# Kernel optimization log

Hardware: AMD Instinct MI355X
Metric: run time of the kernel (lower is better)

## Reference

```python
import jax, jax.numpy as jnp
import numpy as np

B, C, H, W = 32, 48, 64, 128
K = 5  # conv kernel size (1x5 / 5x1)


def _conv1d(x, w, b):
    # x: [B, C, L]; w: [O, I, K]; b: [O]. 'same' conv (pad 2) along L.
    y = jax.lax.conv_general_dilated(x, w, window_strides=(1,), padding=[(2, 2)],
                                     dimension_numbers=("NCH", "OIH", "NCH"))
    return y + b[None, :, None]


def setup_inputs() -> dict:
    key = jax.random.key(0)
    ks = jax.random.split(key, 7)
    s = 0.02  # small init so the 64/128-step linear recurrences stay bounded
    return {
        "x": jax.random.normal(ks[0], (B, C, H, W), dtype=jnp.float32),
        "down_w": jax.random.normal(ks[1], (C, C, K), dtype=jnp.float32) * s,
        "down_b": jax.random.normal(ks[2], (C,), dtype=jnp.float32) * s,
        "right_w": jax.random.normal(ks[3], (C, C, K), dtype=jnp.float32) * s,
        "right_b": jax.random.normal(ks[4], (C,), dtype=jnp.float32) * s,
        "left_w": jax.random.normal(ks[5], (C, C, K), dtype=jnp.float32) * s,
        "left_b": jax.random.normal(ks[6], (C,), dtype=jnp.float32) * s,
    }


def reference(x, down_w, down_b, right_w, right_b, left_w, left_b):
    Bb, Cc, Hh, Ww = x.shape

    def step(w, b):
        def f(carry, inp):
            nxt = inp + _conv1d(carry, w, b)
            return nxt, nxt
        return f

    # --- down pass: d[0]=x[0]; d[t]=x[t]+down_conv(d[t-1]) ---
    xs = jnp.moveaxis(x, 2, 0)                       # [H, B, C, W]
    d0 = xs[0]
    _, d_rest = jax.lax.scan(step(down_w, down_b), d0, xs[1:])
    D = jnp.concatenate([d0[None], d_rest], 0)       # [H, B, C, W]

    # --- up pass: faithfully uses down_conv (source quirk) with index H-3-t
    # u[0]=D[H-1]; u[k]=D[H-2-k]+down_conv(u[k-1]), k=1..H-1 (H-2-k=-1 -> D[H-1])
    seq = jnp.concatenate([D[Hh - 3::-1], D[Hh - 1:Hh]], 0)  # [H-1, B, C, W]
    u0 = D[Hh - 1]
    _, u_rest = jax.lax.scan(step(down_w, down_b), u0, seq)
    U = jnp.concatenate([u0[None], u_rest], 0)[::-1]  # U[i] = u[H-1-i]

    # --- right pass over width: r[0]=U[...,0]; r[t]=U[...,t]+right_conv(r[t-1]) ---
    ws = jnp.moveaxis(jnp.moveaxis(U, 0, 2), 3, 0)   # [W, B, C, H]
    r0 = ws[0]
    _, r_rest = jax.lax.scan(step(right_w, right_b), r0, ws[1:])
    R = jnp.concatenate([r0[None], r_rest], 0)       # [W, B, C, H]

    # --- left pass (reverse): l[0]=R[W-1]; l[k]=R[W-1-k]+left_conv(l[k-1]) ---
    l0 = R[Ww - 1]
    _, l_rest = jax.lax.scan(step(left_w, left_b), l0, R[Ww - 2::-1])
    L = jnp.concatenate([l0[None], l_rest], 0)[::-1]  # [W, B, C, H]

    return jnp.moveaxis(L, 0, 3)                     # [B, C, H, W]
```

## Files before the change

kernel.cpp:

```cpp
#include <hip/hip_runtime.h>
#include <hip/hip_bf16.h>

#define B_ 32
#define C_ 48
#define H_ 64
#define W_ 128
#define K_ 5
#define SLAB (C_*H_*W_)
#define RS 56
#define ROWS 136
#define CBUF (ROWS*RS)
#define WC (W_*C_)
#define HC (H_*C_)
#define KBN 8

typedef __attribute__((ext_vector_type(8))) short short8;
typedef __attribute__((ext_vector_type(4))) float f32x4;

__device__ __forceinline__ void lbar() {
  asm volatile("s_waitcnt lgkmcnt(0)\n\ts_barrier" ::: "memory");
}

__device__ __forceinline__ unsigned short f2bf(float f) {
  union { float f; unsigned u; } v; v.f = f;
  unsigned r = v.u + 0x7fffu + ((v.u >> 16) & 1u);
  return (unsigned short)(r >> 16);
}

__device__ __forceinline__ unsigned pk2(float a, float b) {
  union { __hip_bfloat162 h; unsigned u; } z;
  z.h = __float22bfloat162_rn(float2{a, b});
  return z.u;
}

__device__ __forceinline__ void load_wA(const float* __restrict__ wgt,
                                        const float* __restrict__ bias,
                                        short8 A[3][KBN], f32x4 bv[3],
                                        int l15, int q8, int c0) {
#pragma unroll
  for (int mt = 0; mt < 3; ++mt) {
#pragma unroll
    for (int r = 0; r < 4; ++r) bv[mt][r] = bias[mt * 16 + c0 + r];
#pragma unroll
    for (int kb = 0; kb < KBN; ++kb) {
      short8 f;
#pragma unroll
      for (int j = 0; j < 8; ++j) {
        int kp = kb * 32 + q8 + j;
        int k = kp / 48, i = kp - 48 * k;
        f[j] = (kp < 240)
             ? (short)f2bf(wgt[(mt * 16 + l15) * (C_ * K_) + i * K_ + k])
             : (short)0;
      }
      A[mt][kb] = f;
    }
  }
}

template<int NTW>
__device__ __forceinline__ void load_xin(float4 xv[NTW][3], const float* __restrict__ inp,
                                         size_t lRS, int n0, int l15, int c0) {
#pragma unroll
  for (int nt = 0; nt < NTW; ++nt) {
    const float* p = inp + (size_t)(n0 + nt * 16 + l15) * lRS + c0;
#pragma unroll
    for (int mt = 0; mt < 3; ++mt) xv[nt][mt] = *(const float4*)(p + mt * 16);
  }
}

template<int NTW, int SPL>
__device__ __forceinline__ void do_step(const unsigned short* __restrict__ scr,
                                        unsigned short* __restrict__ scw,
                                        const short8 A[3][KBN], const f32x4 bv[3],
                                        const float4 xv[NTW][3], const int off_r[KBN],
                                        float* __restrict__ outp,
                                        int n0, int l15, int c0) {
  f32x4 acc[SPL][NTW][3];
#pragma unroll
  for (int s = 0; s < SPL; ++s)
#pragma unroll
    for (int nt = 0; nt < NTW; ++nt)
#pragma unroll
      for (int mt = 0; mt < 3; ++mt)
        acc[s][nt][mt] = (s == 0) ? bv[mt] : (f32x4){0.f, 0.f, 0.f, 0.f};

#pragma unroll
  for (int kb = 0; kb < KBN; ++kb) {
    short8 pf[NTW];
#pragma unroll
    for (int nt = 0; nt < NTW; ++nt)
      pf[nt] = *(const short8*)(scr + (size_t)(n0 + nt * 16) * RS + off_r[kb]);
#pragma unroll
    for (int nt = 0; nt < NTW; ++nt)
#pragma unroll
      for (int mt = 0; mt < 3; ++mt)
        acc[kb % SPL][nt][mt] = __builtin_amdgcn_mfma_f32_16x16x32_bf16(
            A[mt][kb], pf[nt], acc[kb % SPL][nt][mt], 0, 0, 0);
  }

#pragma unroll
  for (int nt = 0; nt < NTW; ++nt) {
    const int row = n0 + nt * 16 + l15;
#pragma unroll
    for (int mt = 0; mt < 3; ++mt) {
      f32x4 a = acc[0][nt][mt];
#pragma unroll
      for (int s = 1; s < SPL; ++s)
#pragma unroll
        for (int r = 0; r < 4; ++r) a[r] += acc[s][nt][mt][r];
      float4 v;
      v.x = a[0] + xv[nt][mt].x; v.y = a[1] + xv[nt][mt].y;
      v.z = a[2] + xv[nt][mt].z; v.w = a[3] + xv[nt][mt].w;
      *(float4*)(outp + (size_t)row * C_ + mt * 16 + c0) = v;
      uint2 pk; pk.x = pk2(v.x, v.y); pk.y = pk2(v.z, v.w);
      *(uint2*)(scw + (size_t)(row + 2) * RS + mt * 16 + c0) = pk;
    }
  }
  lbar();
}

template<int NTW>
__device__ __forceinline__ void init_store(unsigned short* __restrict__ scw,
                                           const float* __restrict__ inp, size_t lRS,
                                           float* __restrict__ outp,
                                           int n0, int l15, int c0) {
  float4 xv[NTW][3];
  load_xin<NTW>(xv, inp, lRS, n0, l15, c0);
#pragma unroll
  for (int nt = 0; nt < NTW; ++nt) {
    const int row = n0 + nt * 16 + l15;
#pragma unroll
    for (int mt = 0; mt < 3; ++mt) {
      float4 v = xv[nt][mt];
      *(float4*)(outp + (size_t)row * C_ + mt * 16 + c0) = v;
      uint2 pk; pk.x = pk2(v.x, v.y); pk.y = pk2(v.z, v.w);
      *(uint2*)(scw + (size_t)(row + 2) * RS + mt * 16 + c0) = pk;
    }
  }
  lbar();
}

template<int NTW, int SPL, class FIN, class FOUT>
__device__ __forceinline__ void run_pass(unsigned short* sb, int& p,
                                         const short8 A[3][KBN], const f32x4 bv[3],
                                         const int off_r[KBN],
                                         int nsteps, FIN inadr, size_t lRS, FOUT outadr,
                                         int n0, int l15, int c0) {
  float4 xa[NTW][3], xb[NTW][3];
  load_xin<NTW>(xa, inadr(1), lRS, n0, l15, c0);
  for (int s = 1; s <= nsteps; s += 2) {
    {
      int sn = (s + 1 <= nsteps) ? s + 1 : nsteps;
      load_xin<NTW>(xb, inadr(sn), lRS, n0, l15, c0);
      __builtin_amdgcn_sched_barrier(0x38F);
      do_step<NTW, SPL>(sb + (size_t)p * CBUF, sb + (size_t)(p ^ 1) * CBUF,
                        A, bv, xa, off_r, outadr(s), n0, l15, c0);
      p ^= 1;
    }
    if (s + 1 <= nsteps) {
      int sn = (s + 2 <= nsteps) ? s + 2 : nsteps;
      load_xin<NTW>(xa, inadr(sn), lRS, n0, l15, c0);
      __builtin_amdgcn_sched_barrier(0x38F);
      do_step<NTW, SPL>(sb + (size_t)p * CBUF, sb + (size_t)(p ^ 1) * CBUF,
                        A, bv, xb, off_r, outadr(s + 1), n0, l15, c0);
      p ^= 1;
    }
  }
}

__global__ __launch_bounds__(256, 1) void scnn_mfma(
    float* ws,
    const float* __restrict__ dw, const float* __restrict__ db,
    const float* __restrict__ rw, const float* __restrict__ rb,
    const float* __restrict__ lw, const float* __restrict__ lb,
    float* __restrict__ DU)
{
  __shared__ unsigned short sb[2 * CBUF];
  const int tid = threadIdx.x, lane = tid & 63, wid = tid >> 6;
  const int l15 = lane & 15, q = lane >> 4, q8 = q * 8, c0 = 4 * q;
  const int b = blockIdx.x;
  float* xbuf = ws + (size_t)b * SLAB;
  float* rl   = ws + (size_t)b * SLAB;
  float* du   = DU + (size_t)b * SLAB;
  const int n0w = wid * 32, n0h = wid * 16;

  int off_r[KBN];
#pragma unroll
  for (int kb = 0; kb < KBN; ++kb) {
    int s = kb * 32 + q8;
    int k = s / 48, i0 = s - 48 * k;
    off_r[kb] = (l15 + k) * RS + i0;
  }

  short8 A[3][KBN];
  f32x4 bv[3];
  int p = 0;

  load_wA(dw, db, A, bv, l15, q8, c0);
  { unsigned* z = (unsigned*)sb; for (int i = tid; i < CBUF; i += 256) z[i] = 0u; }
  __syncthreads();
  init_store<2>(sb, xbuf, (size_t)C_, du, n0w, l15, c0);
  run_pass<2, 2>(sb, p, A, bv, off_r, H_ - 1,
                 [&](int s) { return xbuf + (size_t)s * WC; }, (size_t)C_,
                 [&](int s) { return du + (size_t)s * WC; }, n0w, l15, c0);
  __syncthreads();

  run_pass<2, 2>(sb, p, A, bv, off_r, H_ - 1,
                 [&](int s) { int ih = (s <= H_ - 2) ? (H_ - 2 - s) : (H_ - 1);
                              return du + (size_t)ih * WC; }, (size_t)C_,
                 [&](int s) { return du + (size_t)(H_ - 1 - s) * WC; }, n0w, l15, c0);
  __syncthreads();

  load_wA(rw, rb, A, bv, l15, q8, c0);
  { unsigned* z = (unsigned*)sb; for (int i = tid; i < CBUF; i += 256) z[i] = 0u; }
  __syncthreads();
  p = 0;
  init_store<1>(sb, du, (size_t)WC, rl, n0h, l15, c0);
  run_pass<1, 4>(sb, p, A, bv, off_r, W_ - 1,
                 [&](int s) { return du + (size_t)s * C_; }, (size_t)WC,
                 [&](int s) { return rl + (size_t)s * HC; }, n0h, l15, c0);
  __syncthreads();

  load_wA(lw, lb, A, bv, l15, q8, c0);
  run_pass<1, 4>(sb, p, A, bv, off_r, W_ - 1,
                 [&](int s) { return rl + (size_t)(W_ - 1 - s) * HC; }, (size_t)C_,
                 [&](int s) { return rl + (size_t)(W_ - 1 - s) * HC; }, n0h, l15, c0);
}

__global__ __launch_bounds__(256) void xpose_chw_hwc(const float* __restrict__ x,
                                                     float* __restrict__ xT) {
  __shared__ float t[C_ * 129];
  const int bh = blockIdx.x, b = bh >> 6, h = bh & 63;
  const float* src = x + (size_t)b * SLAB + (size_t)h * W_;
  float* dst = xT + (size_t)b * SLAB + (size_t)h * (W_ * C_);
  for (int i = threadIdx.x; i < C_ * W_; i += 256) {
    int c = i >> 7, w = i & 127;
    t[c * 129 + w] = src[(size_t)c * (H_ * W_) + w];
  }
  __syncthreads();
  for (int i = threadIdx.x; i < C_ * W_; i += 256) {
    int w = i / C_, c = i - w * C_;
    dst[i] = t[c * 129 + w];
  }
}

__global__ __launch_bounds__(256) void xpose_whc_chw(const float* __restrict__ L,
                                                     float* __restrict__ out) {
  __shared__ float t[W_ * 49];
  const int bh = blockIdx.x, b = bh >> 6, h = bh & 63;
  const float* src = L + (size_t)b * SLAB + (size_t)h * C_;
  float* dst = out + (size_t)b * SLAB + (size_t)h * W_;
  for (int i = threadIdx.x; i < W_ * C_; i += 256) {
    int w = i / C_, c = i - w * C_;
    t[w * 49 + c] = src[(size_t)w * (H_ * C_) + c];
  }
  __syncthreads();
  for (int i = threadIdx.x; i < C_ * W_; i += 256) {
    int c = i >> 7, w = i & 127;
    dst[(size_t)c * (H_ * W_) + w] = t[w * 49 + c];
  }
}

extern "C" void kernel_launch(void* const* d_in, const int* in_sizes, int n_in,
                              void* d_out, int out_size, void* d_ws, size_t ws_size,
                              hipStream_t stream) {
  const float* x  = (const float*)d_in[0];
  const float* dw = (const float*)d_in[1];
  const float* db = (const float*)d_in[2];
  const float* rw = (const float*)d_in[3];
  const float* rb = (const float*)d_in[4];
  const float* lw = (const float*)d_in[5];
  const float* lb = (const float*)d_in[6];
  float* DU = (float*)d_out;
  float* WS = (float*)d_ws;

  xpose_chw_hwc<<<B_ * H_, 256, 0, stream>>>(x, WS);
  scnn_mfma<<<B_, 256, 0, stream>>>(WS, dw, db, rw, rb, lw, lb, DU);
  xpose_whc_chw<<<B_ * H_, 256, 0, stream>>>(WS, DU);
}
```

Before: 408.8 us.

## Switch recurrence steps to 32x32x16 MFMA with bias folded into constant-one K column

Each recurrence step now uses 32x32x16 bf16 MFMA tiles instead of 16x16x32. The bias is folded into the GEMM as an extra K entry that multiplies a constant-one row in the LDS carry buffer. The width passes split the work across waves by output-channel half and row tile, with two accumulators alternating over K, and the next input load is moved after the MFMA chain. This is meant to cut MFMA issue count and accumulator setup on the serial critical path. In exchange the 48-channel output is padded to 64 rows, which wastes some compute, and the change adds bf16 rounding of the bias.

```diff
diff --git a/kernel.cpp b/kernel.cpp
--- a/kernel.cpp
+++ b/kernel.cpp
@@ -12,10 +12,12 @@
 #define CBUF (ROWS*RS)
 #define WC (W_*C_)
 #define HC (H_*C_)
-#define KBN 8
+#define KBN 16
+#define C1ROW 135
 
 typedef __attribute__((ext_vector_type(8))) short short8;
-typedef __attribute__((ext_vector_type(4))) float f32x4;
+typedef __attribute__((ext_vector_type(16))) float f32x16;
+typedef unsigned short ushort;
 
 __device__ __forceinline__ void lbar() {
   asm volatile("s_waitcnt lgkmcnt(0)\n\ts_barrier" ::: "memory");
@@ -33,139 +35,225 @@
   return z.u;
 }
 
-__device__ __forceinline__ void load_wA(const float* __restrict__ wgt,
-                                        const float* __restrict__ bias,
-                                        short8 A[3][KBN], f32x4 bv[3],
-                                        int l15, int q8, int c0) {
-#pragma unroll
-  for (int mt = 0; mt < 3; ++mt) {
-#pragma unroll
-    for (int r = 0; r < 4; ++r) bv[mt][r] = bias[mt * 16 + c0 + r];
-#pragma unroll
-    for (int kb = 0; kb < KBN; ++kb) {
+template<int NMT>
+__device__ __forceinline__ void load_wA32(const float* __restrict__ wgt,
+                                          const float* __restrict__ bias,
+                                          short8 Aw[NMT][KBN], int mt0,
+                                          int l31, int h) {
+#pragma unroll
+  for (int mti = 0; mti < NMT; ++mti) {
+    const int m = (mt0 + mti) * 32 + l31;
+#pragma unroll
+    for (int kbn = 0; kbn < KBN; ++kbn) {
       short8 f;
 #pragma unroll
       for (int j = 0; j < 8; ++j) {
-        int kp = kb * 32 + q8 + j;
-        int k = kp / 48, i = kp - 48 * k;
-        f[j] = (kp < 240)
-             ? (short)f2bf(wgt[(mt * 16 + l15) * (C_ * K_) + i * K_ + k])
-             : (short)0;
+        int kp = kbn * 16 + h * 8 + j;
+        float val = 0.f;
+        if (m < C_) {
+          if (kp < 240) {
+            int k = kp / 48, i = kp - 48 * k;
+            val = wgt[m * (C_ * K_) + i * K_ + k];
+          } else if (kp == 240) {
+            val = bias[m];
+          }
+        }
+        f[j] = (short)f2bf(val);
       }
-      A[mt][kb] = f;
-    }
-  }
-}
-
-template<int NTW>
-__device__ __forceinline__ void load_xin(float4 xv[NTW][3], const float* __restrict__ inp,
-                                         size_t lRS, int n0, int l15, int c0) {
-#pragma unroll
-  for (int nt = 0; nt < NTW; ++nt) {
-    const float* p = inp + (size_t)(n0 + nt * 16 + l15) * lRS + c0;
-#pragma unroll
-    for (int mt = 0; mt < 3; ++mt) xv[nt][mt] = *(const float4*)(p + mt * 16);
-  }
-}
-
-template<int NTW, int SPL>
-__device__ __forceinline__ void do_step(const unsigned short* __restrict__ scr,
-                                        unsigned short* __restrict__ scw,
-                                        const short8 A[3][KBN], const f32x4 bv[3],
-                                        const float4 xv[NTW][3], const int off_r[KBN],
+      Aw[mti][kbn] = f;
+    }
+  }
+}
+
+__device__ __forceinline__ void loadx6(float4 xv[6], const float* __restrict__ inp,
+                                       size_t inRS, int n0, int l31, int h4) {
+  const float* ip = inp + (size_t)(n0 + l31) * inRS + h4;
+  xv[0] = *(const float4*)(ip + 0);
+  xv[1] = *(const float4*)(ip + 8);
+  xv[2] = *(const float4*)(ip + 16);
+  xv[3] = *(const float4*)(ip + 24);
+  xv[4] = *(const float4*)(ip + 32);
+  xv[5] = *(const float4*)(ip + 40);
+}
+
+__device__ __forceinline__ void stepW32(const ushort* __restrict__ scr,
+                                        ushort* __restrict__ scw,
+                                        const short8 Aw[2][KBN],
+                                        const float4 xvc[6], float4 xvn[6],
+                                        const float* __restrict__ inpn, size_t inRS,
                                         float* __restrict__ outp,
-                                        int n0, int l15, int c0) {
-  f32x4 acc[SPL][NTW][3];
-#pragma unroll
-  for (int s = 0; s < SPL; ++s)
-#pragma unroll
-    for (int nt = 0; nt < NTW; ++nt)
-#pragma unroll
-      for (int mt = 0; mt < 3; ++mt)
-        acc[s][nt][mt] = (s == 0) ? bv[mt] : (f32x4){0.f, 0.f, 0.f, 0.f};
-
-#pragma unroll
-  for (int kb = 0; kb < KBN; ++kb) {
-    short8 pf[NTW];
-#pragma unroll
-    for (int nt = 0; nt < NTW; ++nt)
-      pf[nt] = *(const short8*)(scr + (size_t)(n0 + nt * 16) * RS + off_r[kb]);
-#pragma unroll
-    for (int nt = 0; nt < NTW; ++nt)
-#pragma unroll
-      for (int mt = 0; mt < 3; ++mt)
-        acc[kb % SPL][nt][mt] = __builtin_amdgcn_mfma_f32_16x16x32_bf16(
-            A[mt][kb], pf[nt], acc[kb % SPL][nt][mt], 0, 0, 0);
-  }
-
-#pragma unroll
-  for (int nt = 0; nt < NTW; ++nt) {
-    const int row = n0 + nt * 16 + l15;
-#pragma unroll
-    for (int mt = 0; mt < 3; ++mt) {
-      f32x4 a = acc[0][nt][mt];
-#pragma unroll
-      for (int s = 1; s < SPL; ++s)
-#pragma unroll
-        for (int r = 0; r < 4; ++r) a[r] += acc[s][nt][mt][r];
-      float4 v;
-      v.x = a[0] + xv[nt][mt].x; v.y = a[1] + xv[nt][mt].y;
-      v.z = a[2] + xv[nt][mt].z; v.w = a[3] + xv[nt][mt].w;
-      *(float4*)(outp + (size_t)row * C_ + mt * 16 + c0) = v;
-      uint2 pk; pk.x = pk2(v.x, v.y); pk.y = pk2(v.z, v.w);
-      *(uint2*)(scw + (size_t)(row + 2) * RS + mt * 16 + c0) = pk;
-    }
+                                        int n0, int l31, int h4,
+                                        const int off_r[KBN], int c1off) {
+  f32x16 a0 = (f32x16)(0.0f), a1 = (f32x16)(0.0f);
+  const ushort* bp = scr + (size_t)n0 * RS;
+#pragma unroll
+  for (int kbn = 0; kbn < KBN; ++kbn) {
+    int off = (kbn == 15) ? c1off : off_r[kbn];
+    short8 pf = *(const short8*)(bp + off);
+    a0 = __builtin_amdgcn_mfma_f32_32x32x16_bf16(Aw[0][kbn], pf, a0, 0, 0, 0);
+    a1 = __builtin_amdgcn_mfma_f32_32x32x16_bf16(Aw[1][kbn], pf, a1, 0, 0, 0);
+  }
+  loadx6(xvn, inpn, inRS, n0, l31, h4);
+  __builtin_amdgcn_sched_barrier(0);
+
+  const int row = n0 + l31;
+  float* op = outp + (size_t)row * C_ + h4;
+  ushort* wp = scw + (size_t)(row + 2) * RS + h4;
+#pragma unroll
+  for (int grp = 0; grp < 6; ++grp) {
+    const int g = (grp < 4) ? grp : (grp - 4);
+    const int ch = ((grp < 4) ? 0 : 32) + 8 * g;
+    f32x16 A = (grp < 4) ? a0 : a1;
+    float4 v;
+    v.x = A[4*g+0] + xvc[grp].x; v.y = A[4*g+1] + xvc[grp].y;
+    v.z = A[4*g+2] + xvc[grp].z; v.w = A[4*g+3] + xvc[grp].w;
+    *(float4*)(op + ch) = v;
+    uint2 pk; pk.x = pk2(v.x, v.y); pk.y = pk2(v.z, v.w);
+    *(uint2*)(wp + ch) = pk;
   }
   lbar();
 }
 
-template<int NTW>
-__device__ __forceinline__ void init_store(unsigned short* __restrict__ scw,
-                                           const float* __restrict__ inp, size_t lRS,
-                                           float* __restrict__ outp,
-                                           int n0, int l15, int c0) {
-  float4 xv[NTW][3];
-  load_xin<NTW>(xv, inp, lRS, n0, l15, c0);
-#pragma unroll
-  for (int nt = 0; nt < NTW; ++nt) {
-    const int row = n0 + nt * 16 + l15;
-#pragma unroll
-    for (int mt = 0; mt < 3; ++mt) {
-      float4 v = xv[nt][mt];
-      *(float4*)(outp + (size_t)row * C_ + mt * 16 + c0) = v;
-      uint2 pk; pk.x = pk2(v.x, v.y); pk.y = pk2(v.z, v.w);
-      *(uint2*)(scw + (size_t)(row + 2) * RS + mt * 16 + c0) = pk;
-    }
+template<int MT>
+__device__ __forceinline__ void stepH32(const ushort* __restrict__ scr,
+                                        ushort* __restrict__ scw,
+                                        const short8 Aw[KBN],
+                                        const float4 xvc[4], float4 xvn[4],
+                                        const float* __restrict__ inpn, size_t inRS,
+                                        float* __restrict__ outp,
+                                        int n0, int l31, int h4,
+                                        const int off_r[KBN], int c1off) {
+  constexpr int NG = MT ? 2 : 4;
+  f32x16 a0 = (f32x16)(0.0f), a1 = (f32x16)(0.0f);
+  const ushort* bp = scr + (size_t)n0 * RS;
+#pragma unroll
+  for (int kbn = 0; kbn < KBN; ++kbn) {
+    int off = (kbn == 15) ? c1off : off_r[kbn];
+    short8 pf = *(const short8*)(bp + off);
+    if (kbn & 1) a1 = __builtin_amdgcn_mfma_f32_32x32x16_bf16(Aw[kbn], pf, a1, 0, 0, 0);
+    else         a0 = __builtin_amdgcn_mfma_f32_32x32x16_bf16(Aw[kbn], pf, a0, 0, 0, 0);
+  }
+  const int row = n0 + l31;
+  {
+    const float* ip = inpn + (size_t)row * inRS + MT * 32 + h4;
+#pragma unroll
+    for (int g = 0; g < NG; ++g) xvn[g] = *(const float4*)(ip + 8 * g);
+  }
+  __builtin_amdgcn_sched_barrier(0);
+
+  float* op = outp + (size_t)row * C_ + MT * 32 + h4;
+  ushort* wp = scw + (size_t)(row + 2) * RS + MT * 32 + h4;
+#pragma unroll
+  for (int g = 0; g < NG; ++g) {
+    float4 v;
+    v.x = a0[4*g+0] + a1[4*g+0] + xvc[g].x;
+    v.y = a0[4*g+1] + a1[4*g+1] + xvc[g].y;
+    v.z = a0[4*g+2] + a1[4*g+2] + xvc[g].z;
+    v.w = a0[4*g+3] + a1[4*g+3] + xvc[g].w;
+    *(float4*)(op + 8 * g) = v;
+    uint2 pk; pk.x = pk2(v.x, v.y); pk.y = pk2(v.z, v.w);
+    *(uint2*)(wp + 8 * g) = pk;
   }
   lbar();
 }
 
-template<int NTW, int SPL, class FIN, class FOUT>
-__device__ __forceinline__ void run_pass(unsigned short* sb, int& p,
-                                         const short8 A[3][KBN], const f32x4 bv[3],
-                                         const int off_r[KBN],
-                                         int nsteps, FIN inadr, size_t lRS, FOUT outadr,
-                                         int n0, int l15, int c0) {
-  float4 xa[NTW][3], xb[NTW][3];
-  load_xin<NTW>(xa, inadr(1), lRS, n0, l15, c0);
+__device__ __forceinline__ void initW(ushort* __restrict__ scw,
+                                      const float* __restrict__ inp, size_t inRS,
+                                      float* __restrict__ outp,
+                                      int n0, int l31, int h4) {
+  const int row = n0 + l31;
+  const float* ip = inp + (size_t)row * inRS + h4;
+  float* op = outp + (size_t)row * C_ + h4;
+  ushort* wp = scw + (size_t)(row + 2) * RS + h4;
+#pragma unroll
+  for (int grp = 0; grp < 6; ++grp) {
+    const int g = (grp < 4) ? grp : (grp - 4);
+    const int ch = ((grp < 4) ? 0 : 32) + 8 * g;
+    float4 v = *(const float4*)(ip + ch);
+    *(float4*)(op + ch) = v;
+    uint2 pk; pk.x = pk2(v.x, v.y); pk.y = pk2(v.z, v.w);
+    *(uint2*)(wp + ch) = pk;
+  }
+  lbar();
+}
+
+template<int MT>
+__device__ __forceinline__ void initH(ushort* __restrict__ scw,
+                                      const float* __restrict__ inp, size_t inRS,
+                                      float* __restrict__ outp,
+                                      int n0, int l31, int h4) {
+  constexpr int NG = MT ? 2 : 4;
+  const int row = n0 + l31;
+  const float* ip = inp + (size_t)row * inRS + MT * 32 + h4;
+  float* op = outp + (size_t)row * C_ + MT * 32 + h4;
+  ushort* wp = scw + (size_t)(row + 2) * RS + MT * 32 + h4;
+#pragma unroll
+  for (int g = 0; g < NG; ++g) {
+    float4 v = *(const float4*)(ip + 8 * g);
+    *(float4*)(op + 8 * g) = v;
+    uint2 pk; pk.x = pk2(v.x, v.y); pk.y = pk2(v.z, v.w);
+    *(uint2*)(wp + 8 * g) = pk;
+  }
+  lbar();
+}
+
+template<class FIN, class FOUT>
+__device__ __forceinline__ void run_passW(ushort* sb, int& p,
+                                          const short8 Aw[2][KBN],
+                                          const int off_r[KBN], int c1off,
+                                          int nsteps, FIN inadr, size_t inRS, FOUT outadr,
+                                          int n0, int l31, int h4) {
+  float4 xa[6], xb[6];
+  loadx6(xa, inadr(1), inRS, n0, l31, h4);
   for (int s = 1; s <= nsteps; s += 2) {
     {
       int sn = (s + 1 <= nsteps) ? s + 1 : nsteps;
-      load_xin<NTW>(xb, inadr(sn), lRS, n0, l15, c0);
-      __builtin_amdgcn_sched_barrier(0x38F);
-      do_step<NTW, SPL>(sb + (size_t)p * CBUF, sb + (size_t)(p ^ 1) * CBUF,
-                        A, bv, xa, off_r, outadr(s), n0, l15, c0);
+      stepW32(sb + (size_t)p * CBUF, sb + (size_t)(p ^ 1) * CBUF, Aw, xa, xb,
+              inadr(sn), inRS, outadr(s), n0, l31, h4, off_r, c1off);
       p ^= 1;
     }
     if (s + 1 <= nsteps) {
       int sn = (s + 2 <= nsteps) ? s + 2 : nsteps;
-      load_xin<NTW>(xa, inadr(sn), lRS, n0, l15, c0);
-      __builtin_amdgcn_sched_barrier(0x38F);
-      do_step<NTW, SPL>(sb + (size_t)p * CBUF, sb + (size_t)(p ^ 1) * CBUF,
-                        A, bv, xb, off_r, outadr(s + 1), n0, l15, c0);
+      stepW32(sb + (size_t)p * CBUF, sb + (size_t)(p ^ 1) * CBUF, Aw, xb, xa,
+              inadr(sn), inRS, outadr(s + 1), n0, l31, h4, off_r, c1off);
       p ^= 1;
     }
   }
+}
+
+template<int MT, class FIN, class FOUT>
+__device__ __forceinline__ void run_passH(ushort* sb, int& p,
+                                          const short8 Aw[KBN],
+                                          const int off_r[KBN], int c1off,
+                                          int nsteps, FIN inadr, size_t inRS, FOUT outadr,
+                                          int n0, int l31, int h4) {
+  float4 xa[4], xb[4];
+  {
+    const float* ip = inadr(1) + (size_t)(n0 + l31) * inRS + MT * 32 + h4;
+#pragma unroll
+    for (int g = 0; g < (MT ? 2 : 4); ++g) xa[g] = *(const float4*)(ip + 8 * g);
+  }
+  for (int s = 1; s <= nsteps; s += 2) {
+    {
+      int sn = (s + 1 <= nsteps) ? s + 1 : nsteps;
+      stepH32<MT>(sb + (size_t)p * CBUF, sb + (size_t)(p ^ 1) * CBUF, Aw, xa, xb,
+                  inadr(sn), inRS, outadr(s), n0, l31, h4, off_r, c1off);
+      p ^= 1;
+    }
+    if (s + 1 <= nsteps) {
+      int sn = (s + 2 <= nsteps) ? s + 2 : nsteps;
+      stepH32<MT>(sb + (size_t)p * CBUF, sb + (size_t)(p ^ 1) * CBUF, Aw, xb, xa,
+                  inadr(sn), inRS, outadr(s + 1), n0, l31, h4, off_r, c1off);
+      p ^= 1;
+    }
+  }
+}
+
+__device__ __forceinline__ void zero_carry_c1(ushort* sb, int tid) {
+  unsigned* z = (unsigned*)sb;
+  for (int i = tid; i < CBUF; i += 256) z[i] = 0u;
+  __syncthreads();
+  if (tid == 0) { sb[C1ROW * RS] = 0x3F80; sb[CBUF + C1ROW * RS] = 0x3F80; }
 }
 
 __global__ __launch_bounds__(256, 1) void scnn_mfma(
@@ -175,64 +263,83 @@
     const float* __restrict__ lw, const float* __restrict__ lb,
     float* __restrict__ DU)
 {
-  __shared__ unsigned short sb[2 * CBUF];
+  __shared__ __align__(32) ushort sb[2 * CBUF];
   const int tid = threadIdx.x, lane = tid & 63, wid = tid >> 6;
-  const int l15 = lane & 15, q = lane >> 4, q8 = q * 8, c0 = 4 * q;
+  const int l31 = lane & 31, h = lane >> 5, h4 = h * 4;
   const int b = blockIdx.x;
   float* xbuf = ws + (size_t)b * SLAB;
   float* rl   = ws + (size_t)b * SLAB;
   float* du   = DU + (size_t)b * SLAB;
-  const int n0w = wid * 32, n0h = wid * 16;
 
   int off_r[KBN];
 #pragma unroll
-  for (int kb = 0; kb < KBN; ++kb) {
-    int s = kb * 32 + q8;
+  for (int kbn = 0; kbn < 15; ++kbn) {
+    int s = kbn * 16 + h * 8;
     int k = s / 48, i0 = s - 48 * k;
-    off_r[kb] = (l15 + k) * RS + i0;
-  }
-
-  short8 A[3][KBN];
-  f32x4 bv[3];
+    off_r[kbn] = (l31 + k) * RS + i0;
+  }
+  off_r[15] = 0;
+
+  const int n0w = wid * 32;
+  const int ntH = wid & 1, mtH = wid >> 1;
+  const int n0h = ntH * 32;
+  const int c1w = (C1ROW - n0w) * RS;
+  const int c1h = (C1ROW - n0h) * RS;
+
   int p = 0;
 
-  load_wA(dw, db, A, bv, l15, q8, c0);
-  { unsigned* z = (unsigned*)sb; for (int i = tid; i < CBUF; i += 256) z[i] = 0u; }
-  __syncthreads();
-  init_store<2>(sb, xbuf, (size_t)C_, du, n0w, l15, c0);
-  run_pass<2, 2>(sb, p, A, bv, off_r, H_ - 1,
-                 [&](int s) { return xbuf + (size_t)s * WC; }, (size_t)C_,
-                 [&](int s) { return du + (size_t)s * WC; }, n0w, l15, c0);
-  __syncthreads();
-
-  run_pass<2, 2>(sb, p, A, bv, off_r, H_ - 1,
-                 [&](int s) { int ih = (s <= H_ - 2) ? (H_ - 2 - s) : (H_ - 1);
-                              return du + (size_t)ih * WC; }, (size_t)C_,
-                 [&](int s) { return du + (size_t)(H_ - 1 - s) * WC; }, n0w, l15, c0);
-  __syncthreads();
-
-  load_wA(rw, rb, A, bv, l15, q8, c0);
-  { unsigned* z = (unsigned*)sb; for (int i = tid; i < CBUF; i += 256) z[i] = 0u; }
-  __syncthreads();
-  p = 0;
-  init_store<1>(sb, du, (size_t)WC, rl, n0h, l15, c0);
-  run_pass<1, 4>(sb, p, A, bv, off_r, W_ - 1,
-                 [&](int s) { return du + (size_t)s * C_; }, (size_t)WC,
-                 [&](int s) { return rl + (size_t)s * HC; }, n0h, l15, c0);
-  __syncthreads();
-
-  load_wA(lw, lb, A, bv, l15, q8, c0);
-  run_pass<1, 4>(sb, p, A, bv, off_r, W_ - 1,
-                 [&](int s) { return rl + (size_t)(W_ - 1 - s) * HC; }, (size_t)C_,
-                 [&](int s) { return rl + (size_t)(W_ - 1 - s) * HC; }, n0h, l15, c0);
+  {
+    short8 Aw[2][KBN];
+    load_wA32<2>(dw, db, Aw, 0, l31, h);
+    zero_carry_c1(sb, tid);
+    __syncthreads();
+    initW(sb, xbuf, (size_t)C_, du, n0w, l31, h4);
+    run_passW(sb, p, Aw, off_r, c1w, H_ - 1,
+              [&](int s) { return xbuf + (size_t)s * WC; }, (size_t)C_,
+              [&](int s) { return du + (size_t)s * WC; }, n0w, l31, h4);
+    __syncthreads();
+    run_passW(sb, p, Aw, off_r, c1w, H_ - 1,
+              [&](int s) { int ih = (s <= H_ - 2) ? (H_ - 2 - s) : (H_ - 1);
+                           return du + (size_t)ih * WC; }, (size_t)C_,
+              [&](int s) { return du + (size_t)(H_ - 1 - s) * WC; }, n0w, l31, h4);
+    __syncthreads();
+  }
+
+  {
+    short8 Ah[1][KBN];
+    load_wA32<1>(rw, rb, Ah, mtH, l31, h);
+    zero_carry_c1(sb, tid);
+    __syncthreads();
+    p = 0;
+    if (mtH == 0) initH<0>(sb, du, (size_t)WC, rl, n0h, l31, h4);
+    else          initH<1>(sb, du, (size_t)WC, rl, n0h, l31, h4);
+    if (mtH == 0)
+      run_passH<0>(sb, p, Ah[0], off_r, c1h, W_ - 1,
+                   [&](int s) { return du + (size_t)s * C_; }, (size_t)WC,
+                   [&](int s) { return rl + (size_t)s * HC; }, n0h, l31, h4);
+    else
+      run_passH<1>(sb, p, Ah[0], off_r, c1h, W_ - 1,
+                   [&](int s) { return du + (size_t)s * C_; }, (size_t)WC,
+                   [&](int s) { return rl + (size_t)s * HC; }, n0h, l31, h4);
+    __syncthreads();
+    load_wA32<1>(lw, lb, Ah, mtH, l31, h);
+    if (mtH == 0)
+      run_passH<0>(sb, p, Ah[0], off_r, c1h, W_ - 1,
+                   [&](int s) { return rl + (size_t)(W_ - 1 - s) * HC; }, (size_t)C_,
+                   [&](int s) { return rl + (size_t)(W_ - 1 - s) * HC; }, n0h, l31, h4);
+    else
+      run_passH<1>(sb, p, Ah[0], off_r, c1h, W_ - 1,
+                   [&](int s) { return rl + (size_t)(W_ - 1 - s) * HC; }, (size_t)C_,
+                   [&](int s) { return rl + (size_t)(W_ - 1 - s) * HC; }, n0h, l31, h4);
+  }
 }
 
 __global__ __launch_bounds__(256) void xpose_chw_hwc(const float* __restrict__ x,
                                                      float* __restrict__ xT) {
   __shared__ float t[C_ * 129];
-  const int bh = blockIdx.x, b = bh >> 6, h = bh & 63;
-  const float* src = x + (size_t)b * SLAB + (size_t)h * W_;
-  float* dst = xT + (size_t)b * SLAB + (size_t)h * (W_ * C_);
+  const int bh = blockIdx.x, b = bh >> 6, hh = bh & 63;
+  const float* src = x + (size_t)b * SLAB + (size_t)hh * W_;
+  float* dst = xT + (size_t)b * SLAB + (size_t)hh * (W_ * C_);
   for (int i = threadIdx.x; i < C_ * W_; i += 256) {
     int c = i >> 7, w = i & 127;
     t[c * 129 + w] = src[(size_t)c * (H_ * W_) + w];
@@ -247,9 +354,9 @@
 __global__ __launch_bounds__(256) void xpose_whc_chw(const float* __restrict__ L,
                                                      float* __restrict__ out) {
   __shared__ float t[W_ * 49];
-  const int bh = blockIdx.x, b = bh >> 6, h = bh & 63;
-  const float* src = L + (size_t)b * SLAB + (size_t)h * C_;
-  float* dst = out + (size_t)b * SLAB + (size_t)h * W_;
+  const int bh = blockIdx.x, b = bh >> 6, hh = bh & 63;
+  const float* src = L + (size_t)b * SLAB + (size_t)hh * C_;
+  float* dst = out + (size_t)b * SLAB + (size_t)hh * W_;
   for (int i = threadIdx.x; i < W_ * C_; i += 256) {
     int w = i / C_, c = i - w * C_;
     t[w * 49 + c] = src[(size_t)w * (H_ * C_) + c];
```

Result: slower. 436.8 us (+6.9%).
